# Optimization experiments

Hardware: AMD Instinct MI355X
Metric: run time of the kernel (lower is better)

Reference implementation:

```python
import jax, jax.numpy as jnp
import numpy as np

NMS_THR = 0.7
TOPK = 128      # fixed post-NMS rois per level (static padding for jit)
OUT = 14        # RoIAlign output size
SAMPLES = 2     # samples per bin per dim (fixed approximation of sampling_ratio=-1)
STRIDES = (32.0, 16.0, 8.0)


def get_channel(a):
    # a: [..., 4] boxes as (cx, cy, w, h); FPN level assignment, clamped to [1, 4]
    s = jnp.sqrt(a[..., 2] * a[..., 3])
    return jnp.clip(jnp.floor(3.0 + jnp.log2(s / 224.0)), 1.0, 4.0)


def cxcywh_to_xyxy(b):
    cx, cy, w, h = b[..., 0], b[..., 1], b[..., 2], b[..., 3]
    return jnp.stack([cx - w / 2, cy - h / 2, cx + w / 2, cy + h / 2], axis=-1)


def pairwise_iou(b):
    x1, y1, x2, y2 = b[:, 0], b[:, 1], b[:, 2], b[:, 3]
    area = jnp.maximum(x2 - x1, 0.0) * jnp.maximum(y2 - y1, 0.0)
    ix1 = jnp.maximum(x1[:, None], x1[None, :])
    iy1 = jnp.maximum(y1[:, None], y1[None, :])
    ix2 = jnp.minimum(x2[:, None], x2[None, :])
    iy2 = jnp.minimum(y2[:, None], y2[None, :])
    inter = jnp.maximum(ix2 - ix1, 0.0) * jnp.maximum(iy2 - iy1, 0.0)
    union = area[:, None] + area[None, :] - inter
    return inter / jnp.maximum(union, 1e-9)


def nms_keep(boxes_xyxy, scores, thr):
    # Greedy NMS over masked scores (-inf entries sort last and are excluded later).
    n = scores.shape[0]
    order = jnp.argsort(-scores)
    iou = pairwise_iou(boxes_xyxy[order])  # [N, N]
    idx = jnp.arange(n)

    def body(sup, i):
        keep_i = ~sup[i]
        sup = sup | (keep_i & (iou[i] > thr) & (idx > i))
        return sup, keep_i

    _, keeps_sorted = jax.lax.scan(body, jnp.zeros(n, dtype=bool), idx)
    return jnp.zeros(n, dtype=bool).at[order].set(keeps_sorted)


def roi_align(feat, boxes):
    # feat: [C, H, W]; boxes: [K, 4]. NOTE: the original prepare_boxes feeds
    # (cx, cy, w, h) straight into RoIAlign, which interprets them as
    # (x1, y1, x2, y2) -- replicated faithfully here. spatial_scale = 1.
    C, H, W = feat.shape
    K = boxes.shape[0]
    x1, y1, x2, y2 = boxes[:, 0], boxes[:, 1], boxes[:, 2], boxes[:, 3]
    rw = jnp.maximum(x2 - x1, 1.0)
    rh = jnp.maximum(y2 - y1, 1.0)
    bw = rw / OUT
    bh = rh / OUT
    # fractional bin offsets, [OUT*SAMPLES]
    f = (jnp.arange(OUT, dtype=feat.dtype)[:, None]
         + (jnp.arange(SAMPLES, dtype=feat.dtype)[None, :] + 0.5) / SAMPLES).reshape(-1)
    ys = y1[:, None] + bh[:, None] * f[None, :]  # [K, S]
    xs = x1[:, None] + bw[:, None] * f[None, :]
    Y = ys[:, :, None]  # [K, S, 1]
    X = xs[:, None, :]  # [K, 1, S]
    valid = (Y > -1.0) & (Y < H) & (X > -1.0) & (X < W)  # [K, S, S]
    Yc = jnp.clip(Y, 0.0, H - 1.0)
    Xc = jnp.clip(X, 0.0, W - 1.0)
    y0 = jnp.floor(Yc)
    x0 = jnp.floor(Xc)
    y0i = y0.astype(jnp.int32)
    x0i = x0.astype(jnp.int32)
    y1i = jnp.minimum(y0i + 1, H - 1)
    x1i = jnp.minimum(x0i + 1, W - 1)
    ly = Yc - y0
    lx = Xc - x0
    hy = 1.0 - ly
    hx = 1.0 - lx
    g = lambda yi, xi: feat[:, yi, xi]  # -> [C, K, S, S]
    val = (g(y0i, x0i) * (hy * hx) + g(y0i, x1i) * (hy * lx)
           + g(y1i, x0i) * (ly * hx) + g(y1i, x1i) * (ly * lx))
    val = val * valid.astype(val.dtype)
    val = val.reshape(C, K, OUT, SAMPLES, OUT, SAMPLES).mean(axis=(3, 5))
    return jnp.transpose(val, (1, 0, 2, 3))  # [K, C, OUT, OUT]


def level_extract(feat, boxes, scores, levs, nl):
    # one image, one target FPN level: mask, NMS, fixed top-K select, RoIAlign
    mask = levs == nl
    msc = jnp.where(mask, scores, -jnp.inf)
    xyxy = cxcywh_to_xyxy(boxes)
    keep = nms_keep(jax.lax.stop_gradient(xyxy), jax.lax.stop_gradient(msc), NMS_THR)
    eff = jnp.where(keep & mask, msc, -jnp.inf)
    vals, sel = jax.lax.top_k(jax.lax.stop_gradient(eff), TOPK)
    valid = jnp.isfinite(vals)
    rois = boxes[sel] * valid[:, None].astype(boxes.dtype)
    out = roi_align(feat, rois)
    return out * valid[:, None, None, None].astype(out.dtype)


def _forward(p32, p16, p8, p4, a32, a16, a8, s32, s16, s8):
    anchors = (a32, a16, a8)  # p4 proposals are computed then discarded in the
    # original (grouping loop only runs l in range(3)); p4 features are never
    # RoIAligned either (nl loops 1..3), so p4 only appears as an unused input.
    levs = jnp.concatenate([get_channel(a) for a in anchors], axis=1)      # [B, N]
    boxes = jnp.concatenate([a * s for a, s in zip(anchors, STRIDES)], axis=1)
    scores = jnp.concatenate([s32, s16, s8], axis=1)
    outs = []
    for nl, feat in zip((1.0, 2.0, 3.0), (p32, p16, p8)):
        fn = jax.vmap(lambda f, b, s, l, nl=nl: level_extract(f, b, s, l, nl))
        outs.append(fn(feat, boxes, scores, levs))  # [B, TOPK, C, 14, 14]
    return jnp.concatenate(outs, axis=1)  # [B, 3*TOPK, C, 14, 14]


def setup_inputs():
    key = jax.random.key(0)
    ks = jax.random.split(key, 10)
    B, C = 2, 256
    p32 = jax.random.normal(ks[0], (B, C, 32, 32), jnp.float32)
    p16 = jax.random.normal(ks[1], (B, C, 64, 64), jnp.float32)
    p8 = jax.random.normal(ks[2], (B, C, 128, 128), jnp.float32)
    p4 = jax.random.normal(ks[3], (B, C, 256, 256), jnp.float32)

    def mk_anchors(k, n, hf):
        k1, k2 = jax.random.split(k)
        cxy = jax.random.uniform(k1, (B, n, 2), jnp.float32) * hf
        wh = 16.0 + jax.random.uniform(k2, (B, n, 2), jnp.float32) * 434.0
        return jnp.concatenate([cxy, wh], axis=-1)

    anchors_32 = mk_anchors(ks[4], 512, 32.0)
    anchors_16 = mk_anchors(ks[5], 1024, 64.0)
    anchors_8 = mk_anchors(ks[6], 2048, 128.0)
    scores_32 = jax.random.normal(ks[7], (B, 512), jnp.float32)
    scores_16 = jax.random.normal(ks[8], (B, 1024), jnp.float32)
    scores_8 = jax.random.normal(ks[9], (B, 2048), jnp.float32)
    return dict(p32=p32, p16=p16, p8=p8, p4=p4,
                anchors_32=anchors_32, anchors_16=anchors_16, anchors_8=anchors_8,
                scores_32=scores_32, scores_16=scores_16, scores_8=scores_8)


def reference(p32, p16, p8, p4, anchors_32, anchors_16, anchors_8,
              scores_32, scores_16, scores_8):
    return _forward(p32, p16, p8, p4, anchors_32, anchors_16, anchors_8,
                    scores_32, scores_16, scores_8)
```

## Files before the change

kernel.cpp:

```cpp
#include <hip/hip_runtime.h>
#include <stdint.h>

#define NMS_THR 0.7f
#define TOPK 128
#define NTOT 3584
#define CAP 2048
#define CHUNK 256
#define OUTSZ 14
#define NSAMP 28

typedef unsigned long long u64;
typedef float vf4 __attribute__((ext_vector_type(4)));
typedef float float2u __attribute__((ext_vector_type(2), aligned(4)));

__device__ __forceinline__ u64 shfl_xor64(u64 v, int mask) {
    int lo = __shfl_xor((int)(unsigned)v, mask);
    int hi = __shfl_xor((int)(v >> 32), mask);
    return ((u64)(unsigned)hi << 32) | (unsigned)lo;
}
__device__ __forceinline__ void cex_shfl(u64 &e, int t, int j, int k) {
    u64 p = shfl_xor64(e, j);
    bool up = ((t & k) == 0);
    bool lower = ((t & j) == 0);
    u64 mn = (e < p) ? e : p;
    u64 mx = (e < p) ? p : e;
    e = (lower == up) ? mn : mx;
}
__device__ __forceinline__ float boxarea(float4 b) {
    return __fmul_rn(fmaxf(__fsub_rn(b.z, b.x), 0.0f),
                     fmaxf(__fsub_rn(b.w, b.y), 0.0f));
}
__device__ __forceinline__ bool iou_gt(float4 a, float aa, float4 b, float ba) {
    float i1 = fmaxf(a.x, b.x), i2 = fmaxf(a.y, b.y);
    float i3 = fminf(a.z, b.z), i4 = fminf(a.w, b.w);
    float inr = __fmul_rn(fmaxf(__fsub_rn(i3, i1), 0.0f),
                          fmaxf(__fsub_rn(i4, i2), 0.0f));
    float unr = __fsub_rn(__fadd_rn(aa, ba), inr);
    return __fdiv_rn(inr, fmaxf(unr, 1e-9f)) > NMS_THR;
}

__device__ __forceinline__ void fetch_anchor(
    const float* __restrict__ a32, const float* __restrict__ a16,
    const float* __restrict__ a8,
    const float* __restrict__ s32, const float* __restrict__ s16,
    const float* __restrict__ s8,
    int b, int i, float* A, float* st, float* sc)
{
    const float* P;
    if (i < 512) {
        P = a32 + (b * 512 + i) * 4;  *st = 32.0f; *sc = s32[b * 512 + i];
    } else if (i < 1536) {
        int j = i - 512;
        P = a16 + (b * 1024 + j) * 4; *st = 16.0f; *sc = s16[b * 1024 + j];
    } else {
        int j = i - 1536;
        P = a8 + (b * 2048 + j) * 4;  *st = 8.0f;  *sc = s8[b * 2048 + j];
    }
    float4 v = *(const float4*)P;
    A[0] = v.x; A[1] = v.y; A[2] = v.z; A[3] = v.w;
}

__global__ __launch_bounds__(1024) void select_kernel(
    const float* __restrict__ a32, const float* __restrict__ a16,
    const float* __restrict__ a8,
    const float* __restrict__ s32, const float* __restrict__ s16,
    const float* __restrict__ s8,
    float* __restrict__ rois,
    int* __restrict__ validOut)
{
    __shared__ u64 keys[CAP];
    __shared__ float4 cbox4[CAP];
    __shared__ float4 kb4[TOPK];
    __shared__ float karea[TOPK];
    __shared__ u64 extw[16];
    __shared__ int selList[TOPK];
    __shared__ int mCount, keptSh;

    int prob = blockIdx.x;
    int b = prob / 3;
    int nl = prob % 3 + 1;
    int tid = threadIdx.x;
    int lane = tid & 63;
    int wv = tid >> 6;
    int t0 = (wv << 7) + lane;
    int t1 = t0 + 64;

    if (tid == 0) mCount = 0;
    __syncthreads();

    for (int i = tid; i < NTOT; i += 1024) {
        float A[4], st, sc;
        fetch_anchor(a32, a16, a8, s32, s16, s8, b, i, A, &st, &sc);
        float s = sqrtf(__fmul_rn(A[2], A[3]));
        float lv = floorf(__fadd_rn(3.0f, log2f(__fdiv_rn(s, 224.0f))));
        lv = fminf(fmaxf(lv, 1.0f), 4.0f);
        bool sel = ((int)lv == nl);
        u64 bal = __ballot(sel);
        if (bal) {
            int pos0;
            if (lane == 0) pos0 = atomicAdd(&mCount, __popcll(bal));
            pos0 = __shfl(pos0, 0);
            if (sel) {
                unsigned u = __float_as_uint(sc);
                u = (u & 0x80000000u) ? ~u : (u | 0x80000000u);
                unsigned d = ~u;
                int pos = pos0 + __popcll(bal & ((1ull << lane) - 1ull));
                if (pos < CAP) keys[pos] = ((u64)d << 32) | (unsigned)i;
            }
        }
    }
    __syncthreads();
    int m = mCount;
    if (m > CAP) m = CAP;
    for (int i = m + tid; i < CAP; i += 1024) keys[i] = ~0ull;
    __syncthreads();

    {
        u64 e0 = keys[t0], e1 = keys[t1];
        for (int k = 2; k <= 128; k <<= 1) {
            int jstart = k >> 1;
            if (k == 128) {
                bool up = ((t0 & k) == 0);
                if ((e0 > e1) == up) { u64 tmp = e0; e0 = e1; e1 = tmp; }
                jstart = 32;
            }
            for (int j = jstart; j > 0; j >>= 1) {
                cex_shfl(e0, t0, j, k);
                cex_shfl(e1, t1, j, k);
            }
        }
        keys[t0] = e0; keys[t1] = e1;
    }
    __syncthreads();
    for (int k = 256; k <= 2048; k <<= 1) {
        for (int j = k >> 1; j >= 128; j >>= 1) {
            for (int t = tid; t < CAP; t += 1024) {
                int ixj = t ^ j;
                if (ixj > t) {
                    u64 a = keys[t], bb = keys[ixj];
                    bool up = ((t & k) == 0);
                    if ((a > bb) == up) { keys[t] = bb; keys[ixj] = a; }
                }
            }
            __syncthreads();
        }
        {
            u64 e0 = keys[t0], e1 = keys[t1];
            bool up = ((t0 & k) == 0);
            if ((e0 > e1) == up) { u64 tmp = e0; e0 = e1; e1 = tmp; }
            for (int j = 32; j > 0; j >>= 1) {
                cex_shfl(e0, t0, j, k);
                cex_shfl(e1, t1, j, k);
            }
            keys[t0] = e0; keys[t1] = e1;
        }
        __syncthreads();
    }

    for (int r = tid; r < m; r += 1024) {
        int orig = (int)(keys[r] & 0xffffffffu);
        float A[4], st, sc;
        fetch_anchor(a32, a16, a8, s32, s16, s8, b, orig, A, &st, &sc);
        float cx = A[0] * st, cy = A[1] * st, w = A[2] * st, h = A[3] * st;
        float4 v;
        v.x = __fsub_rn(cx, 0.5f * w);
        v.y = __fsub_rn(cy, 0.5f * h);
        v.z = __fadd_rn(cx, 0.5f * w);
        v.w = __fadd_rn(cy, 0.5f * h);
        cbox4[r] = v;
    }
    __syncthreads();

    int kept = 0;
    int g = wv & 3;
    int ksub = wv >> 2;
    for (int base = 0; base < m && kept < TOPK; base += CHUNK) {
        int n = m - base; if (n > CHUNK) n = CHUNK;

        int c = g * 64 + lane;
        bool cv = c < n;
        float4 cb = cbox4[base + (cv ? c : 0)];
        float car = boxarea(cb);
        bool s = false;
        for (int kk = ksub; kk < kept; kk += 4) {
            if (iou_gt(kb4[kk], karea[kk], cb, car)) s = true;
        }
        u64 bal = __ballot(s && cv);
        if (lane == 0) extw[wv] = bal;
        __syncthreads();

        if (wv == 0) {
            u64 e0 = extw[0] | extw[4] | extw[8]  | extw[12];
            u64 e1 = extw[1] | extw[5] | extw[9]  | extw[13];
            u64 e2 = extw[2] | extw[6] | extw[10] | extw[14];
            u64 e3 = extw[3] | extw[7] | extw[11] | extw[15];
            int c0 = lane, c1 = 64 + lane, c2 = 128 + lane, c3 = 192 + lane;
            float4 B0 = cbox4[base + (c0 < n ? c0 : 0)];
            float4 B1 = cbox4[base + (c1 < n ? c1 : 0)];
            float4 B2 = cbox4[base + (c2 < n ? c2 : 0)];
            float4 B3 = cbox4[base + (c3 < n ? c3 : 0)];
            float a0 = boxarea(B0), a1 = boxarea(B1);
            float a2 = boxarea(B2), a3 = boxarea(B3);
            bool al0 = (c0 < n) && !((e0 >> lane) & 1ull);
            bool al1 = (c1 < n) && !((e1 >> lane) & 1ull);
            bool al2 = (c2 < n) && !((e2 >> lane) & 1ull);
            bool al3 = (c3 < n) && !((e3 >> lane) & 1ull);
            int nk = kept;
            while (nk < TOPK) {
                u64 b0 = __ballot(al0);
                u64 b1 = __ballot(al1);
                u64 b2 = __ballot(al2);
                u64 b3 = __ballot(al3);
                int j;
                if (b0)      j = __builtin_ctzll(b0);
                else if (b1) j = 64 + __builtin_ctzll(b1);
                else if (b2) j = 128 + __builtin_ctzll(b2);
                else if (b3) j = 192 + __builtin_ctzll(b3);
                else break;
                float4 pb = cbox4[base + j];
                float par = boxarea(pb);
                if (lane == 0) {
                    selList[nk] = base + j;
                    kb4[nk] = pb; karea[nk] = par;
                }
                al0 = al0 && (c0 != j) && !((c0 > j) && iou_gt(pb, par, B0, a0));
                al1 = al1 && (c1 != j) && !((c1 > j) && iou_gt(pb, par, B1, a1));
                al2 = al2 && (c2 != j) && !((c2 > j) && iou_gt(pb, par, B2, a2));
                al3 = al3 && (c3 != j) && !((c3 > j) && iou_gt(pb, par, B3, a3));
                nk++;
            }
            if (lane == 0) keptSh = nk;
        }
        __syncthreads();
        kept = keptSh;
    }

    for (int k = tid; k < TOPK; k += 1024) {
        float4 rv = make_float4(0.0f, 0.0f, 0.0f, 0.0f);
        int vld = 0;
        if (k < kept) {
            int orig = (int)(keys[selList[k]] & 0xffffffffu);
            float A[4], st, sc;
            fetch_anchor(a32, a16, a8, s32, s16, s8, b, orig, A, &st, &sc);
            rv = make_float4(A[0] * st, A[1] * st, A[2] * st, A[3] * st);
            vld = 1;
        }
        ((float4*)rois)[prob * TOPK + k] = rv;
        validOut[prob * TOPK + k] = vld;
    }
}

__global__ __launch_bounds__(256) void roialign_kernel(
    const float* __restrict__ p32, const float* __restrict__ p16,
    const float* __restrict__ p8,
    const float* __restrict__ rois, const int* __restrict__ validIn,
    float* __restrict__ out)
{
    int roiIdx = blockIdx.x;
    int b = roiIdx / 384;
    int slot = roiIdx - b * 384;
    int lvl = slot / TOPK;
    int k = slot - lvl * TOPK;
    int prob = b * 3 + lvl;
    int tid = threadIdx.x;

    int vld = validIn[prob * TOPK + k];
    if (!vld) return;

    float* O = out + (size_t)roiIdx * 256 * 196;

    int W;
    const float* feat;
    if (lvl == 0)      { W = 32;  feat = p32; }
    else if (lvl == 1) { W = 64;  feat = p16; }
    else               { W = 128; feat = p8; }
    int HW = W * W;
    const float* F0 = feat + (size_t)b * 256 * HW;

    __shared__ int sxb[NSAMP], sy0[NSAMP], sy1[NSAMP];
    __shared__ float swx0[NSAMP], swx1[NSAMP], shy[NSAMP], sly[NSAMP];
    __shared__ int sxv[NSAMP], syv[NSAMP];
    __shared__ int oiL[OUTSZ], ojL[OUTSZ];
    __shared__ int nyx[2];

    if (tid < 2 * NSAMP) {
        const float* R = rois + ((size_t)prob * TOPK + k) * 4;
        float x1 = R[0], y1 = R[1], x2 = R[2], y2 = R[3];
        float rw = fmaxf(__fsub_rn(x2, x1), 1.0f);
        float rh = fmaxf(__fsub_rn(y2, y1), 1.0f);
        float bw = __fdiv_rn(rw, 14.0f);
        float bh = __fdiv_rn(rh, 14.0f);
        int axis = tid / NSAMP;
        int s = tid - axis * NSAMP;
        float fi = (float)(s >> 1) + ((s & 1) ? 0.75f : 0.25f);
        float start = axis ? y1 : x1;
        float bsz = axis ? bh : bw;
        float lim = (float)W;
        float X = __fadd_rn(start, __fmul_rn(bsz, fi));
        bool v = (X > -1.0f) && (X < lim);
        float Xc = fminf(fmaxf(X, 0.0f), lim - 1.0f);
        float x0f = floorf(Xc);
        int x0 = (int)x0f;
        float l = __fsub_rn(Xc, x0f);
        float hh = __fsub_rn(1.0f, l);
        float vf = v ? 1.0f : 0.0f;
        if (axis == 0) {
            int base; float w0, w1;
            if (x0 >= W - 1) { base = W - 2; w0 = 0.0f; w1 = vf; }
            else             { base = x0;    w0 = hh * vf; w1 = l * vf; }
            sxb[s] = base; swx0[s] = w0; swx1[s] = w1; sxv[s] = v ? 1 : 0;
        } else {
            sy0[s] = x0; sy1[s] = min(x0 + 1, W - 1);
            shy[s] = hh * vf; sly[s] = l * vf; syv[s] = v ? 1 : 0;
        }
    }
    __syncthreads();

    if (tid == 0) {
        int n = 0;
        for (int oi = 0; oi < OUTSZ; oi++)
            if (syv[2 * oi] | syv[2 * oi + 1]) oiL[n++] = oi;
        nyx[0] = n;
    }
    if (tid == 1) {
        int n = 0;
        for (int oj = 0; oj < OUTSZ; oj++)
            if (sxv[2 * oj] | sxv[2 * oj + 1]) ojL[n++] = oj;
        nyx[1] = n;
    }
    __syncthreads();

    int ny = nyx[0], nx = nyx[1];
    int total = ny * nx;
    if (total == 0) return;

    int w = tid >> 6;
    int lane = tid & 63;

    for (int ci = w; ci < total; ci += 4) {
        int oi = oiL[ci / nx];
        int oj = ojL[ci - (ci / nx) * nx];
        int sA = oi * 2, sB = sA + 1;
        int tA = oj * 2, tB = tA + 1;
        int y0A = sy0[sA], y1A = sy1[sA], y0B = sy0[sB], y1B = sy1[sB];
        float hyA = shy[sA], lyA = sly[sA], hyB = shy[sB], lyB = sly[sB];
        int xA = sxb[tA], xB = sxb[tB];
        float xw0A = swx0[tA], xw1A = swx1[tA];
        float xw0B = swx0[tB], xw1B = swx1[tB];
        int p = oi * 14 + oj;

        for (int it = 0; it < 4; it++) {
            int c = lane + it * 64;
            const float* F = F0 + c * HW;
            const float* rA0 = F + y0A * W;
            const float* rA1 = F + y1A * W;
            const float* rB0 = F + y0B * W;
            const float* rB1 = F + y1B * W;

            float2u a0 = *(const float2u*)(rA0 + xA);
            float2u a1 = *(const float2u*)(rA1 + xA);
            float2u c0 = *(const float2u*)(rA0 + xB);
            float2u c1 = *(const float2u*)(rA1 + xB);
            float2u b0 = *(const float2u*)(rB0 + xA);
            float2u b1 = *(const float2u*)(rB1 + xA);
            float2u d0 = *(const float2u*)(rB0 + xB);
            float2u d1 = *(const float2u*)(rB1 + xB);

            float s00 = hyA * (xw0A * a0.x + xw1A * a0.y) + lyA * (xw0A * a1.x + xw1A * a1.y);
            float s01 = hyA * (xw0B * c0.x + xw1B * c0.y) + lyA * (xw0B * c1.x + xw1B * c1.y);
            float s10 = hyB * (xw0A * b0.x + xw1A * b0.y) + lyB * (xw0A * b1.x + xw1A * b1.y);
            float s11 = hyB * (xw0B * d0.x + xw1B * d0.y) + lyB * (xw0B * d1.x + xw1B * d1.y);
            O[c * 196 + p] = 0.25f * (s00 + s01 + s10 + s11);
        }
    }
}

extern "C" void kernel_launch(void* const* d_in, const int* in_sizes, int n_in,
                              void* d_out, int out_size, void* d_ws, size_t ws_size,
                              hipStream_t stream) {
    const float* p32 = (const float*)d_in[0];
    const float* p16 = (const float*)d_in[1];
    const float* p8  = (const float*)d_in[2];
    const float* a32 = (const float*)d_in[4];
    const float* a16 = (const float*)d_in[5];
    const float* a8  = (const float*)d_in[6];
    const float* s32 = (const float*)d_in[7];
    const float* s16 = (const float*)d_in[8];
    const float* s8  = (const float*)d_in[9];
    float* out = (float*)d_out;

    const size_t totalFloats = 3072 + 768;

    float* base;
    if (ws_size >= totalFloats * 4) {
        base = (float*)d_ws;
    } else {
        base = (float*)d_in[3];
    }
    float* rois  = base;
    int*   valid = (int*)(base + 3072);

    hipMemsetAsync(out, 0, out_size, stream);
    select_kernel<<<6, 1024, 0, stream>>>(a32, a16, a8, s32, s16, s8,
                                          rois, valid);
    roialign_kernel<<<768, 256, 0, stream>>>(p32, p16, p8, rois, valid, out);
}
```

Measured before the change: 359.9 us.

## Shrink select block, precompute chunk suppression bitmasks, fold output zeroing into RoIAlign

The select kernel drops to 512 threads with four keys per thread in the bitonic sort, so more of the sort stays in registers. Greedy NMS now works on 64-candidate chunks: each wave precomputes intra-chunk IoU suppression bitmasks in shared memory, so the serial loop in wave 0 only does bitmask ops instead of IoU math per pick. The separate hipMemsetAsync over the whole output is removed and each RoIAlign block zeroes its own output slice, which saves a launch but also writes every valid slice twice. Smaller chunks mean more block-wide barriers and more iterations of the outer chunk loop.

```diff
diff --git a/kernel.cpp b/kernel.cpp
--- a/kernel.cpp
+++ b/kernel.cpp
@@ -5,7 +5,6 @@
 #define TOPK 128
 #define NTOT 3584
 #define CAP 2048
-#define CHUNK 256
 #define OUTSZ 14
 #define NSAMP 28
 
@@ -25,6 +24,10 @@
     u64 mn = (e < p) ? e : p;
     u64 mx = (e < p) ? p : e;
     e = (lower == up) ? mn : mx;
+}
+__device__ __forceinline__ void cex_reg(u64 &a, u64 &b, int t, int k) {
+    bool up = ((t & k) == 0);
+    if ((a > b) == up) { u64 x = a; a = b; b = x; }
 }
 __device__ __forceinline__ float boxarea(float4 b) {
     return __fmul_rn(fmaxf(__fsub_rn(b.z, b.x), 0.0f),
@@ -60,7 +63,7 @@
     A[0] = v.x; A[1] = v.y; A[2] = v.z; A[3] = v.w;
 }
 
-__global__ __launch_bounds__(1024) void select_kernel(
+__global__ __launch_bounds__(512) void select_kernel(
     const float* __restrict__ a32, const float* __restrict__ a16,
     const float* __restrict__ a8,
     const float* __restrict__ s32, const float* __restrict__ s16,
@@ -72,7 +75,8 @@
     __shared__ float4 cbox4[CAP];
     __shared__ float4 kb4[TOPK];
     __shared__ float karea[TOPK];
-    __shared__ u64 extw[16];
+    __shared__ u64 supRow[64];
+    __shared__ u64 extw[8];
     __shared__ int selList[TOPK];
     __shared__ int mCount, keptSh;
 
@@ -82,13 +86,12 @@
     int tid = threadIdx.x;
     int lane = tid & 63;
     int wv = tid >> 6;
-    int t0 = (wv << 7) + lane;
-    int t1 = t0 + 64;
+    int t0 = (wv << 8) + lane;
 
     if (tid == 0) mCount = 0;
     __syncthreads();
 
-    for (int i = tid; i < NTOT; i += 1024) {
+    for (int i = tid; i < NTOT; i += 512) {
         float A[4], st, sc;
         fetch_anchor(a32, a16, a8, s32, s16, s8, b, i, A, &st, &sc);
         float s = sqrtf(__fmul_rn(A[2], A[3]));
@@ -112,29 +115,29 @@
     __syncthreads();
     int m = mCount;
     if (m > CAP) m = CAP;
-    for (int i = m + tid; i < CAP; i += 1024) keys[i] = ~0ull;
+    for (int i = m + tid; i < CAP; i += 512) keys[i] = ~0ull;
     __syncthreads();
 
     {
-        u64 e0 = keys[t0], e1 = keys[t1];
-        for (int k = 2; k <= 128; k <<= 1) {
-            int jstart = k >> 1;
-            if (k == 128) {
-                bool up = ((t0 & k) == 0);
-                if ((e0 > e1) == up) { u64 tmp = e0; e0 = e1; e1 = tmp; }
-                jstart = 32;
-            }
-            for (int j = jstart; j > 0; j >>= 1) {
-                cex_shfl(e0, t0, j, k);
-                cex_shfl(e1, t1, j, k);
-            }
-        }
-        keys[t0] = e0; keys[t1] = e1;
-    }
-    __syncthreads();
-    for (int k = 256; k <= 2048; k <<= 1) {
-        for (int j = k >> 1; j >= 128; j >>= 1) {
-            for (int t = tid; t < CAP; t += 1024) {
+        u64 e0 = keys[t0], e1 = keys[t0 + 64], e2 = keys[t0 + 128], e3 = keys[t0 + 192];
+        for (int k = 2; k <= 256; k <<= 1) {
+            for (int j = k >> 1; j > 0; j >>= 1) {
+                if (j == 128) {
+                    cex_reg(e0, e2, t0, k); cex_reg(e1, e3, t0 + 64, k);
+                } else if (j == 64) {
+                    cex_reg(e0, e1, t0, k); cex_reg(e2, e3, t0 + 128, k);
+                } else {
+                    cex_shfl(e0, t0, j, k);        cex_shfl(e1, t0 + 64, j, k);
+                    cex_shfl(e2, t0 + 128, j, k);  cex_shfl(e3, t0 + 192, j, k);
+                }
+            }
+        }
+        keys[t0] = e0; keys[t0 + 64] = e1; keys[t0 + 128] = e2; keys[t0 + 192] = e3;
+    }
+    __syncthreads();
+    for (int k = 512; k <= 2048; k <<= 1) {
+        for (int j = k >> 1; j >= 256; j >>= 1) {
+            for (int t = tid; t < CAP; t += 512) {
                 int ixj = t ^ j;
                 if (ixj > t) {
                     u64 a = keys[t], bb = keys[ixj];
@@ -145,19 +148,19 @@
             __syncthreads();
         }
         {
-            u64 e0 = keys[t0], e1 = keys[t1];
-            bool up = ((t0 & k) == 0);
-            if ((e0 > e1) == up) { u64 tmp = e0; e0 = e1; e1 = tmp; }
+            u64 e0 = keys[t0], e1 = keys[t0 + 64], e2 = keys[t0 + 128], e3 = keys[t0 + 192];
+            cex_reg(e0, e2, t0, k); cex_reg(e1, e3, t0 + 64, k);
+            cex_reg(e0, e1, t0, k); cex_reg(e2, e3, t0 + 128, k);
             for (int j = 32; j > 0; j >>= 1) {
-                cex_shfl(e0, t0, j, k);
-                cex_shfl(e1, t1, j, k);
-            }
-            keys[t0] = e0; keys[t1] = e1;
+                cex_shfl(e0, t0, j, k);        cex_shfl(e1, t0 + 64, j, k);
+                cex_shfl(e2, t0 + 128, j, k);  cex_shfl(e3, t0 + 192, j, k);
+            }
+            keys[t0] = e0; keys[t0 + 64] = e1; keys[t0 + 128] = e2; keys[t0 + 192] = e3;
         }
         __syncthreads();
     }
 
-    for (int r = tid; r < m; r += 1024) {
+    for (int r = tid; r < m; r += 512) {
         int orig = (int)(keys[r] & 0xffffffffu);
         float A[4], st, sc;
         fetch_anchor(a32, a16, a8, s32, s16, s8, b, orig, A, &st, &sc);
@@ -172,61 +175,47 @@
     __syncthreads();
 
     int kept = 0;
-    int g = wv & 3;
-    int ksub = wv >> 2;
-    for (int base = 0; base < m && kept < TOPK; base += CHUNK) {
-        int n = m - base; if (n > CHUNK) n = CHUNK;
-
-        int c = g * 64 + lane;
-        bool cv = c < n;
-        float4 cb = cbox4[base + (cv ? c : 0)];
+    for (int base = 0; base < m && kept < TOPK; base += 64) {
+        int n = m - base; if (n > 64) n = 64;
+        bool cv = lane < n;
+        float4 cb = cbox4[base + (cv ? lane : 0)];
         float car = boxarea(cb);
+
         bool s = false;
-        for (int kk = ksub; kk < kept; kk += 4) {
+        for (int kk = wv; kk < kept; kk += 8)
             if (iou_gt(kb4[kk], karea[kk], cb, car)) s = true;
-        }
-        u64 bal = __ballot(s && cv);
-        if (lane == 0) extw[wv] = bal;
+        u64 balA = __ballot(s && cv);
+        if (lane == 0) extw[wv] = balA;
+
+        #pragma unroll
+        for (int r = 0; r < 8; r++) {
+            int i = (wv << 3) + r;
+            if (i < n) {
+                float4 ib = cbox4[base + i];
+                float iar = boxarea(ib);
+                bool bit = cv && (lane > i) && iou_gt(ib, iar, cb, car);
+                u64 bal = __ballot(bit);
+                if (lane == 0) supRow[i] = bal;
+            }
+        }
         __syncthreads();
 
         if (wv == 0) {
-            u64 e0 = extw[0] | extw[4] | extw[8]  | extw[12];
-            u64 e1 = extw[1] | extw[5] | extw[9]  | extw[13];
-            u64 e2 = extw[2] | extw[6] | extw[10] | extw[14];
-            u64 e3 = extw[3] | extw[7] | extw[11] | extw[15];
-            int c0 = lane, c1 = 64 + lane, c2 = 128 + lane, c3 = 192 + lane;
-            float4 B0 = cbox4[base + (c0 < n ? c0 : 0)];
-            float4 B1 = cbox4[base + (c1 < n ? c1 : 0)];
-            float4 B2 = cbox4[base + (c2 < n ? c2 : 0)];
-            float4 B3 = cbox4[base + (c3 < n ? c3 : 0)];
-            float a0 = boxarea(B0), a1 = boxarea(B1);
-            float a2 = boxarea(B2), a3 = boxarea(B3);
-            bool al0 = (c0 < n) && !((e0 >> lane) & 1ull);
-            bool al1 = (c1 < n) && !((e1 >> lane) & 1ull);
-            bool al2 = (c2 < n) && !((e2 >> lane) & 1ull);
-            bool al3 = (c3 < n) && !((e3 >> lane) & 1ull);
+            u64 ext = extw[0] | extw[1] | extw[2] | extw[3]
+                    | extw[4] | extw[5] | extw[6] | extw[7];
+            bool alive = cv && !((ext >> lane) & 1ull);
             int nk = kept;
             while (nk < TOPK) {
-                u64 b0 = __ballot(al0);
-                u64 b1 = __ballot(al1);
-                u64 b2 = __ballot(al2);
-                u64 b3 = __ballot(al3);
-                int j;
-                if (b0)      j = __builtin_ctzll(b0);
-                else if (b1) j = 64 + __builtin_ctzll(b1);
-                else if (b2) j = 128 + __builtin_ctzll(b2);
-                else if (b3) j = 192 + __builtin_ctzll(b3);
-                else break;
-                float4 pb = cbox4[base + j];
-                float par = boxarea(pb);
-                if (lane == 0) {
-                    selList[nk] = base + j;
-                    kb4[nk] = pb; karea[nk] = par;
+                u64 bal = __ballot(alive);
+                if (bal == 0ull) break;
+                int pick = __builtin_ctzll(bal);
+                u64 prow = supRow[pick];
+                if (lane == 0) selList[nk] = base + pick;
+                if (lane == 1) {
+                    float4 pb = cbox4[base + pick];
+                    kb4[nk] = pb; karea[nk] = boxarea(pb);
                 }
-                al0 = al0 && (c0 != j) && !((c0 > j) && iou_gt(pb, par, B0, a0));
-                al1 = al1 && (c1 != j) && !((c1 > j) && iou_gt(pb, par, B1, a1));
-                al2 = al2 && (c2 != j) && !((c2 > j) && iou_gt(pb, par, B2, a2));
-                al3 = al3 && (c3 != j) && !((c3 > j) && iou_gt(pb, par, B3, a3));
+                alive = alive && (lane != pick) && !((prow >> lane) & 1ull);
                 nk++;
             }
             if (lane == 0) keptSh = nk;
@@ -235,7 +224,7 @@
         kept = keptSh;
     }
 
-    for (int k = tid; k < TOPK; k += 1024) {
+    for (int k = tid; k < TOPK; k += 512) {
         float4 rv = make_float4(0.0f, 0.0f, 0.0f, 0.0f);
         int vld = 0;
         if (k < kept) {
@@ -264,10 +253,14 @@
     int prob = b * 3 + lvl;
     int tid = threadIdx.x;
 
+    float* O = out + (size_t)roiIdx * 256 * 196;
+
+    vf4 z = (vf4)0.0f;
+    vf4* O4 = (vf4*)O;
+    for (int i = tid; i < 12544; i += 256) O4[i] = z;
+
     int vld = validIn[prob * TOPK + k];
     if (!vld) return;
-
-    float* O = out + (size_t)roiIdx * 256 * 196;
 
     int W;
     const float* feat;
@@ -400,8 +393,7 @@
     float* rois  = base;
     int*   valid = (int*)(base + 3072);
 
-    hipMemsetAsync(out, 0, out_size, stream);
-    select_kernel<<<6, 1024, 0, stream>>>(a32, a16, a8, s32, s16, s8,
-                                          rois, valid);
+    select_kernel<<<6, 512, 0, stream>>>(a32, a16, a8, s32, s16, s8,
+                                         rois, valid);
     roialign_kernel<<<768, 256, 0, stream>>>(p32, p16, p8, rois, valid, out);
 }
```

After: 394.5 us. 1.1x slower.
